# Kernel tuning notes

Hardware: AMD Instinct MI355X
Metric: run time of the kernel (lower is better)

Reference implementation:

```python
import jax, jax.numpy as jnp
from jax import lax
import numpy as np


def _gru_layer(x_seq, W_ih, W_hh, b_ih, b_hh):
    """Single GRU layer, torch gate ordering (r, z, n). x_seq: [B, T, I].
    Returns (all hidden states [B, T, H], final hidden [B, H])."""
    B, T, _ = x_seq.shape
    H = W_hh.shape[1]
    # Precompute input projections for all timesteps: [B, T, 3H]
    x_proj = jnp.einsum('bti,gi->btg', x_seq, W_ih) + b_ih

    def step(h, xp):
        hp = h @ W_hh.T + b_hh                       # [B, 3H]
        xr, xz, xn = jnp.split(xp, 3, axis=-1)
        hr, hz, hn = jnp.split(hp, 3, axis=-1)
        r = jax.nn.sigmoid(xr + hr)
        z = jax.nn.sigmoid(xz + hz)
        n = jnp.tanh(xn + r * hn)
        h_new = (1.0 - z) * n + z * h
        return h_new, h_new

    h0 = jnp.zeros((B, H), dtype=x_seq.dtype)
    hT, hs = lax.scan(step, h0, x_proj.transpose(1, 0, 2))  # scan over time
    return hs.transpose(1, 0, 2), hT


def setup_inputs() -> dict:
    key = jax.random.key(0)
    ks = jax.random.split(key, 12)
    B, T, I, H, O = 128, 1000, 64, 512, 1
    s_in = 1.0 / np.sqrt(H)  # torch GRU init scale
    d = {
        'x': jax.random.normal(ks[0], (B, T, I), jnp.float32),
        'W_ih0': jax.random.uniform(ks[1], (3 * H, I), jnp.float32, -s_in, s_in),
        'W_hh0': jax.random.uniform(ks[2], (3 * H, H), jnp.float32, -s_in, s_in),
        'b_ih0': jax.random.uniform(ks[3], (3 * H,), jnp.float32, -s_in, s_in),
        'b_hh0': jax.random.uniform(ks[4], (3 * H,), jnp.float32, -s_in, s_in),
        'W_ih1': jax.random.uniform(ks[5], (3 * H, H), jnp.float32, -s_in, s_in),
        'W_hh1': jax.random.uniform(ks[6], (3 * H, H), jnp.float32, -s_in, s_in),
        'b_ih1': jax.random.uniform(ks[7], (3 * H,), jnp.float32, -s_in, s_in),
        'b_hh1': jax.random.uniform(ks[8], (3 * H,), jnp.float32, -s_in, s_in),
        'W_fc': jax.random.uniform(ks[9], (O, H), jnp.float32, -s_in, s_in),
        'b_fc': jax.random.uniform(ks[10], (O,), jnp.float32, -s_in, s_in),
    }
    return d


def reference(x, W_ih0, W_hh0, b_ih0, b_hh0, W_ih1, W_hh1, b_ih1, b_hh1, W_fc, b_fc):
    # Layer 0 (eval mode: inter-layer dropout is identity)
    h_seq0, _ = _gru_layer(x, W_ih0, W_hh0, b_ih0, b_hh0)
    # Layer 1; final hidden state of the last layer is h_n[-1]
    _, hT1 = _gru_layer(h_seq0, W_ih1, W_hh1, b_ih1, b_hh1)
    out = hT1 @ W_fc.T + b_fc          # [B, O]
    return jax.nn.sigmoid(out)
```

## Files before the change

kernel.cpp:

```cpp
#include <hip/hip_runtime.h>

typedef unsigned int u32;
typedef unsigned short u16;
typedef short bf16x8 __attribute__((ext_vector_type(8)));
typedef float f32x4 __attribute__((ext_vector_type(4)));

#define TLEN 1000
#define BATCH 128
#define IDIM 64
#define HDIM 512

#define NWG 256
#define NTHR 256

#define H0_OFF 0
#define H1_OFF 262144
#define PX0_OFF 525312
#define PH0_OFF 721920
#define PX1_OFF 2294784
#define PH1_OFF 3867648
#define FLG_OFF 5440512
#define XSL_OFF 5442560

__device__ __forceinline__ u16 f2bf(float f) {
  u32 u = __float_as_uint(f);
  u += 0x7fffu + ((u >> 16) & 1u);
  return (u16)(u >> 16);
}
__device__ __forceinline__ float bf2f(u16 h) { return __uint_as_float(((u32)h) << 16); }
__device__ __forceinline__ float sigm(float x) { return 1.0f / (1.0f + __expf(-x)); }
__device__ __forceinline__ float tanhfast(float x) {
  float e = __expf(-2.0f * fabsf(x));
  float t = (1.0f - e) / (1.0f + e);
  return x >= 0.0f ? t : -t;
}
__device__ __forceinline__ u32 umin2(u32 a, u32 b) { return a < b ? a : b; }
__device__ __forceinline__ u32 umax2(u32 a, u32 b) { return a > b ? a : b; }

__device__ __forceinline__ void sys_st16(u16* p, u32 v) {
  asm volatile("global_store_short %0, %1, off sc0 sc1" ::"v"(p), "v"(v) : "memory");
}
__device__ __forceinline__ void sys_st32(u32* p, u32 v) {
  asm volatile("global_store_dword %0, %1, off sc0 sc1" ::"v"(p), "v"(v) : "memory");
}
__device__ __forceinline__ uint4 sys_ld128(const u32* p) {
  uint4 v;
  asm volatile("global_load_dwordx4 %0, %1, off sc0 sc1\n\ts_waitcnt vmcnt(0)"
               : "=v"(v) : "v"(p) : "memory");
  return v;
}
__device__ __forceinline__ void sys_ldA(bf16x8& d, const u16* p) {
  asm volatile("global_load_dwordx4 %0, %1, off sc0 sc1" : "=v"(d) : "v"(p));
}
__device__ __forceinline__ void dev_st32(u32* p, u32 v) {
  asm volatile("global_store_dword %0, %1, off sc1" ::"v"(p), "v"(v) : "memory");
}
__device__ __forceinline__ uint4 dev_ld128(const u32* p) {
  uint4 v;
  asm volatile("global_load_dwordx4 %0, %1, off sc1\n\ts_waitcnt vmcnt(0)"
               : "=v"(v) : "v"(p) : "memory");
  return v;
}
__device__ __forceinline__ void l2_st16(u16* p, u32 v) {
  asm volatile("global_store_short %0, %1, off sc0" ::"v"(p), "v"(v) : "memory");
}
__device__ __forceinline__ void l2_ldA(bf16x8& d, const u16* p) {
  asm volatile("global_load_dwordx4 %0, %1, off sc0" : "=v"(d) : "v"(p));
}

__global__ void pack_weights(const float* Wih0, const float* Whh0,
                             const float* Wih1, const float* Whh1, char* ws) {
  int fid = blockIdx.x * NTHR + threadIdx.x;
  const float* src;
  int K, Kks;
  size_t obase;
  int f = fid;
  if (f < 12288) {
    src = Wih0; K = 64; Kks = 2; obase = PX0_OFF;
  } else if (f < 12288 + 98304) {
    f -= 12288; src = Whh0; K = 512; Kks = 16; obase = PH0_OFF;
  } else if (f < 12288 + 2 * 98304) {
    f -= 12288 + 98304; src = Wih1; K = 512; Kks = 16; obase = PX1_OFF;
  } else if (f < 12288 + 3 * 98304) {
    f -= 12288 + 2 * 98304; src = Whh1; K = 512; Kks = 16; obase = PH1_OFF;
  } else {
    return;
  }
  int lane = f & 63;
  int r = f >> 6;
  int ks = r % Kks; r /= Kks;
  int ct = r % 3;
  int sl = r / 3;
  int grow = ct * 512 + sl * 16 + (lane & 15);
  int k = ks * 32 + ((lane >> 4) * 8);
  const float* s = src + (size_t)grow * K + k;
  u32 p0 = f2bf(s[0]) | ((u32)f2bf(s[1]) << 16);
  u32 p1 = f2bf(s[2]) | ((u32)f2bf(s[3]) << 16);
  u32 p2 = f2bf(s[4]) | ((u32)f2bf(s[5]) << 16);
  u32 p3 = f2bf(s[6]) | ((u32)f2bf(s[7]) << 16);
  *(uint4*)(ws + obase + (size_t)f * 16) = make_uint4(p0, p1, p2, p3);
}

__device__ __forceinline__ void fast_barrier(u32* flagsS, u32* flagsD, int fidx, u32 target) {
  __syncthreads();
  if (threadIdx.x == 0) {
    asm volatile("s_waitcnt vmcnt(0)" ::: "memory");
    dev_st32(flagsD + fidx, target);
    sys_st32(flagsS + fidx, target);
  }
  if (threadIdx.x < 64) {
    const int lane = threadIdx.x;
    for (;;) {
      u32 m = 0xFFFFFFFFu;
      if (lane < 8) {
        uint4 v = sys_ld128(flagsS + lane * 4);
        m = umin2(umin2(v.x, v.y), umin2(v.z, v.w));
      } else if (lane < 16) {
        uint4 v = dev_ld128(flagsD + (lane - 8) * 4);
        m = umin2(umin2(v.x, v.y), umin2(v.z, v.w));
      }
      m = umax2(m, __shfl_xor(m, 8));
      m = umin2(m, __shfl_xor(m, 1));
      m = umin2(m, __shfl_xor(m, 2));
      m = umin2(m, __shfl_xor(m, 4));
      if (__shfl(m, 0) >= target) break;
      __builtin_amdgcn_s_sleep(2);
    }
  }
  __syncthreads();
}

struct KP {
  const float *x, *bih0, *bhh0, *bih1, *bhh1, *Wfc, *bfc;
  float* out;
  char* ws;
};

#define MFMA(A, B, C) __builtin_amdgcn_mfma_f32_16x16x32_bf16((A), (B), (C), 0, 0, 0)

__global__ __launch_bounds__(NTHR, 1) void gru_main(KP P) {
  __shared__ f32x4 red[4][8][64];
  const int tid = threadIdx.x;
  const int lane = tid & 63;
  const int w = tid >> 6;
  const int b = blockIdx.x;
  const int bg = b & 7;
  const int q = b >> 3;
  const int layer = q & 1;
  const int colWG = q >> 1;

  char* ws = P.ws;
  u16* h0 = (u16*)(ws + H0_OFF);
  u16* h1 = (u16*)(ws + H1_OFF);
  u32* flagsS = (u32*)(ws + FLG_OFF) + bg * 64;
  u32* xslot = (u32*)(ws + XSL_OFF) + bg * 64;
  u32* flagsD = xslot + 32;
  const bf16x8* px = (const bf16x8*)(ws + (layer ? PX1_OFF : PX0_OFF));
  const bf16x8* ph = (const bf16x8*)(ws + (layer ? PH1_OFF : PH0_OFF));

  const float* bih = layer ? P.bih1 : P.bih0;
  const float* bhh = layer ? P.bhh1 : P.bhh0;
  const int cw = w & 1;
  const int jcol = colWG * 32 + cw * 16 + (lane & 15);
  const float b_r = bih[jcol] + bhh[jcol];
  const float b_z = bih[HDIM + jcol] + bhh[HDIM + jcol];
  const float b_nx = bih[2 * HDIM + jcol];
  const float b_nh = bhh[2 * HDIM + jcol];

  u16* hout = layer ? h1 : h0;
  const size_t bgoff = (size_t)bg * 16 * HDIM;

  bf16x8 xB[3][2][4], hB[3][2][4];
#pragma unroll
  for (int ct = 0; ct < 3; ++ct)
#pragma unroll
    for (int cs = 0; cs < 2; ++cs)
#pragma unroll
      for (int j = 0; j < 4; ++j)
        hB[ct][cs][j] =
            ph[((size_t)((colWG * 2 + cs) * 3 + ct) * 16 + (j * 4 + w)) * 64 + lane];
  if (layer == 0) {
    const bf16x8 z8 = {0, 0, 0, 0, 0, 0, 0, 0};
#pragma unroll
    for (int ct = 0; ct < 3; ++ct)
#pragma unroll
      for (int cs = 0; cs < 2; ++cs)
#pragma unroll
        for (int j = 0; j < 4; ++j) xB[ct][cs][j] = z8;
    if (w < 2) {
#pragma unroll
      for (int ct = 0; ct < 3; ++ct)
#pragma unroll
        for (int cs = 0; cs < 2; ++cs)
          xB[ct][cs][0] = px[((size_t)((colWG * 2 + cs) * 3 + ct) * 2 + w) * 64 + lane];
    }
  } else {
#pragma unroll
    for (int ct = 0; ct < 3; ++ct)
#pragma unroll
      for (int cs = 0; cs < 2; ++cs)
#pragma unroll
        for (int j = 0; j < 4; ++j)
          xB[ct][cs][j] =
              px[((size_t)((colWG * 2 + cs) * 3 + ct) * 16 + (j * 4 + w)) * 64 + lane];
  }

  u32 xcc = 0;
  asm volatile("s_getreg_b32 %0, hwreg(HW_REG_XCC_ID)" : "=s"(xcc));
  if (tid == 0) sys_st32(xslot + q, xcc + 1u);
  fast_barrier(flagsS, flagsD, q, 1u);
  u32 mn = 0xFFFFFFFFu, mx = 0u;
  if (lane < 8) {
    uint4 v = sys_ld128(xslot + lane * 4);
    mn = umin2(umin2(v.x, v.y), umin2(v.z, v.w));
    mx = umax2(umax2(v.x, v.y), umax2(v.z, v.w));
  }
  mn = umin2(mn, __shfl_xor(mn, 1)); mx = umax2(mx, __shfl_xor(mx, 1));
  mn = umin2(mn, __shfl_xor(mn, 2)); mx = umax2(mx, __shfl_xor(mx, 2));
  mn = umin2(mn, __shfl_xor(mn, 4)); mx = umax2(mx, __shfl_xor(mx, 4));
  mn = __shfl(mn, 0); mx = __shfl(mx, 0);
  const bool isLocal = (mn != 0u) && (mn == mx);

  const f32x4 zf = {0.f, 0.f, 0.f, 0.f};
  f32x4 hown = zf;

#pragma unroll 1
  for (int tick = 0; tick <= TLEN; ++tick) {
    const int p = tick & 1;
    const bool active = (layer == 0) ? (tick < TLEN) : (tick >= 1);
    if (active) {
      f32x4 aR[2], aZ[2], aXN[2], aHN[2];
#pragma unroll
      for (int cs = 0; cs < 2; ++cs) { aR[cs] = zf; aZ[cs] = zf; aXN[cs] = zf; aHN[cs] = zf; }
      const u16* h0src = h0 + (size_t)(1 - p) * BATCH * HDIM + bgoff;

      if (layer == 0) {
        if (w < 2) {
          const float* s = P.x +
              ((size_t)(bg * 16 + (lane & 15)) * TLEN + tick) * IDIM +
              w * 32 + ((lane >> 4) * 8);
          float4 v0 = ((const float4*)s)[0];
          float4 v1 = ((const float4*)s)[1];
          bf16x8 A;
          A[0] = (short)f2bf(v0.x); A[1] = (short)f2bf(v0.y);
          A[2] = (short)f2bf(v0.z); A[3] = (short)f2bf(v0.w);
          A[4] = (short)f2bf(v1.x); A[5] = (short)f2bf(v1.y);
          A[6] = (short)f2bf(v1.z); A[7] = (short)f2bf(v1.w);
#pragma unroll
          for (int cs = 0; cs < 2; ++cs) {
            aR[cs] = MFMA(A, xB[0][cs][0], aR[cs]);
            aZ[cs] = MFMA(A, xB[1][cs][0], aZ[cs]);
            aXN[cs] = MFMA(A, xB[2][cs][0], aXN[cs]);
          }
        }
        bf16x8 A[4];
        if (isLocal) {
#pragma unroll
          for (int j = 0; j < 4; ++j)
            l2_ldA(A[j], h0src + (size_t)(lane & 15) * HDIM + (j * 4 + w) * 32 +
                             ((lane >> 4) * 8));
        } else {
#pragma unroll
          for (int j = 0; j < 4; ++j)
            sys_ldA(A[j], h0src + (size_t)(lane & 15) * HDIM + (j * 4 + w) * 32 +
                              ((lane >> 4) * 8));
        }
        asm volatile("s_waitcnt vmcnt(0)" ::: "memory");
        __builtin_amdgcn_sched_barrier(0);
#pragma unroll
        for (int j = 0; j < 4; ++j)
#pragma unroll
          for (int cs = 0; cs < 2; ++cs) {
            aR[cs] = MFMA(A[j], hB[0][cs][j], aR[cs]);
            aZ[cs] = MFMA(A[j], hB[1][cs][j], aZ[cs]);
            aHN[cs] = MFMA(A[j], hB[2][cs][j], aHN[cs]);
          }
      } else {
        const u16* h1src = h1 + (size_t)(1 - p) * BATCH * HDIM + bgoff;
        bf16x8 A1[4], A2[4];
        if (isLocal) {
#pragma unroll
          for (int j = 0; j < 4; ++j) {
            const size_t off = (size_t)(lane & 15) * HDIM + (j * 4 + w) * 32 +
                               ((lane >> 4) * 8);
            l2_ldA(A1[j], h0src + off);
            l2_ldA(A2[j], h1src + off);
          }
        } else {
#pragma unroll
          for (int j = 0; j < 4; ++j) {
            const size_t off = (size_t)(lane & 15) * HDIM + (j * 4 + w) * 32 +
                               ((lane >> 4) * 8);
            sys_ldA(A1[j], h0src + off);
            sys_ldA(A2[j], h1src + off);
          }
        }
        asm volatile("s_waitcnt vmcnt(0)" ::: "memory");
        __builtin_amdgcn_sched_barrier(0);
#pragma unroll
        for (int j = 0; j < 4; ++j)
#pragma unroll
          for (int cs = 0; cs < 2; ++cs) {
            aR[cs] = MFMA(A1[j], xB[0][cs][j], aR[cs]);
            aZ[cs] = MFMA(A1[j], xB[1][cs][j], aZ[cs]);
            aXN[cs] = MFMA(A1[j], xB[2][cs][j], aXN[cs]);
          }
#pragma unroll
        for (int j = 0; j < 4; ++j)
#pragma unroll
          for (int cs = 0; cs < 2; ++cs) {
            aR[cs] = MFMA(A2[j], hB[0][cs][j], aR[cs]);
            aZ[cs] = MFMA(A2[j], hB[1][cs][j], aZ[cs]);
            aHN[cs] = MFMA(A2[j], hB[2][cs][j], aHN[cs]);
          }
      }

#pragma unroll
      for (int cs = 0; cs < 2; ++cs) {
        red[w][0 + cs][lane] = aR[cs];
        red[w][2 + cs][lane] = aZ[cs];
        red[w][4 + cs][lane] = aXN[cs];
        red[w][6 + cs][lane] = aHN[cs];
      }
      __syncthreads();
      f32x4 R = zf, Z = zf, XN = zf, HN = zf;
#pragma unroll
      for (int kq = 0; kq < 4; ++kq) {
        R = R + red[kq][0 + cw][lane];
        Z = Z + red[kq][2 + cw][lane];
        XN = XN + red[kq][4 + cw][lane];
        HN = HN + red[kq][6 + cw][lane];
      }

      if (w < 2) {
        u16* hw = hout + (size_t)p * BATCH * HDIM;
        u32 hv16[4];
        int rowb[4];
#pragma unroll
        for (int qq = 0; qq < 4; ++qq) {
          float r = sigm(R[qq] + b_r);
          float z = sigm(Z[qq] + b_z);
          float n = tanhfast(XN[qq] + b_nx + r * (HN[qq] + b_nh));
          float hv = (1.f - z) * n + z * hown[qq];
          hown[qq] = hv;
          hv16[qq] = (u32)f2bf(hv);
          rowb[qq] = bg * 16 + (lane >> 4) * 4 + qq;
        }
        if (isLocal) {
#pragma unroll
          for (int qq = 0; qq < 4; ++qq)
            l2_st16(&hw[(size_t)rowb[qq] * HDIM + jcol], hv16[qq]);
        } else {
#pragma unroll
          for (int qq = 0; qq < 4; ++qq)
            sys_st16(&hw[(size_t)rowb[qq] * HDIM + jcol], hv16[qq]);
        }
      }
    }
    fast_barrier(flagsS, flagsD, q, (u32)(tick + 2));
  }

  if (layer == 1 && colWG == 0) {
    const u16* hT = h1;
    int row = tid >> 4, qq = tid & 15;
    const u16* hr = hT + (size_t)(bg * 16 + row) * HDIM + qq * 32;
    bf16x8 hv[4];
    if (isLocal) {
#pragma unroll
      for (int c = 0; c < 4; ++c) l2_ldA(hv[c], hr + c * 8);
    } else {
#pragma unroll
      for (int c = 0; c < 4; ++c) sys_ldA(hv[c], hr + c * 8);
    }
    asm volatile("s_waitcnt vmcnt(0)" ::: "memory");
    const float* wf = P.Wfc + qq * 32;
    float s = 0.f;
#pragma unroll
    for (int c = 0; c < 4; ++c)
#pragma unroll
      for (int k = 0; k < 8; ++k) s += bf2f((u16)hv[c][k]) * wf[c * 8 + k];
    s += __shfl_xor(s, 1);
    s += __shfl_xor(s, 2);
    s += __shfl_xor(s, 4);
    s += __shfl_xor(s, 8);
    if (qq == 0) P.out[bg * 16 + row] = sigm(s + P.bfc[0]);
  }
}

extern "C" void kernel_launch(void* const* d_in, const int* in_sizes, int n_in,
                              void* d_out, int out_size, void* d_ws, size_t ws_size,
                              hipStream_t stream) {
  const float* x = (const float*)d_in[0];
  const float* Wih0 = (const float*)d_in[1];
  const float* Whh0 = (const float*)d_in[2];
  const float* bih0 = (const float*)d_in[3];
  const float* bhh0 = (const float*)d_in[4];
  const float* Wih1 = (const float*)d_in[5];
  const float* Whh1 = (const float*)d_in[6];
  const float* bih1 = (const float*)d_in[7];
  const float* bhh1 = (const float*)d_in[8];
  const float* Wfc = (const float*)d_in[9];
  const float* bfc = (const float*)d_in[10];

  hipMemsetAsync(d_ws, 0, 524288, stream);
  hipMemsetAsync((char*)d_ws + FLG_OFF, 0, 4096, stream);
  pack_weights<<<dim3(1200), dim3(NTHR), 0, stream>>>(Wih0, Whh0, Wih1, Whh1, (char*)d_ws);

  KP P = {x, bih0, bhh0, bih1, bhh1, Wfc, bfc, (float*)d_out, (char*)d_ws};
  void* args[] = {&P};
  hipError_t ce = hipLaunchCooperativeKernel((void*)gru_main, dim3(NWG), dim3(NTHR), args, 0,
                                             stream);
  if (ce != hipSuccess) {
    (void)hipGetLastError();
    gru_main<<<dim3(NWG), dim3(NTHR), 0, stream>>>(P);
  }
}
```

Baseline: 4.031 ms.

## Replace per-tick group barrier with per-producer progress flags and 4-slot hidden ring

Result: faster. 3.876 ms (-3.8%).

```diff
diff --git a/kernel.cpp b/kernel.cpp
--- a/kernel.cpp
+++ b/kernel.cpp
@@ -14,13 +14,13 @@
 #define NTHR 256
 
 #define H0_OFF 0
-#define H1_OFF 262144
-#define PX0_OFF 525312
-#define PH0_OFF 721920
-#define PX1_OFF 2294784
-#define PH1_OFF 3867648
-#define FLG_OFF 5440512
-#define XSL_OFF 5442560
+#define H1_OFF 524288
+#define PX0_OFF 1048576
+#define PH0_OFF 1245184
+#define PX1_OFF 2818048
+#define PH1_OFF 4390912
+#define FLG_OFF 5963776
+#define XSL_OFF 5967872
 
 __device__ __forceinline__ u16 f2bf(float f) {
   u32 u = __float_as_uint(f);
@@ -52,17 +52,17 @@
 __device__ __forceinline__ void sys_ldA(bf16x8& d, const u16* p) {
   asm volatile("global_load_dwordx4 %0, %1, off sc0 sc1" : "=v"(d) : "v"(p));
 }
-__device__ __forceinline__ void dev_st32(u32* p, u32 v) {
-  asm volatile("global_store_dword %0, %1, off sc1" ::"v"(p), "v"(v) : "memory");
-}
-__device__ __forceinline__ uint4 dev_ld128(const u32* p) {
+__device__ __forceinline__ void l2_st16(u16* p, u32 v) {
+  asm volatile("global_store_short %0, %1, off sc0" ::"v"(p), "v"(v) : "memory");
+}
+__device__ __forceinline__ void l2_st32(u32* p, u32 v) {
+  asm volatile("global_store_dword %0, %1, off sc0" ::"v"(p), "v"(v) : "memory");
+}
+__device__ __forceinline__ uint4 l2_ld128(const u32* p) {
   uint4 v;
-  asm volatile("global_load_dwordx4 %0, %1, off sc1\n\ts_waitcnt vmcnt(0)"
+  asm volatile("global_load_dwordx4 %0, %1, off sc0\n\ts_waitcnt vmcnt(0)"
                : "=v"(v) : "v"(p) : "memory");
   return v;
-}
-__device__ __forceinline__ void l2_st16(u16* p, u32 v) {
-  asm volatile("global_store_short %0, %1, off sc0" ::"v"(p), "v"(v) : "memory");
 }
 __device__ __forceinline__ void l2_ldA(bf16x8& d, const u16* p) {
   asm volatile("global_load_dwordx4 %0, %1, off sc0" : "=v"(d) : "v"(p));
@@ -101,35 +101,6 @@
   *(uint4*)(ws + obase + (size_t)f * 16) = make_uint4(p0, p1, p2, p3);
 }
 
-__device__ __forceinline__ void fast_barrier(u32* flagsS, u32* flagsD, int fidx, u32 target) {
-  __syncthreads();
-  if (threadIdx.x == 0) {
-    asm volatile("s_waitcnt vmcnt(0)" ::: "memory");
-    dev_st32(flagsD + fidx, target);
-    sys_st32(flagsS + fidx, target);
-  }
-  if (threadIdx.x < 64) {
-    const int lane = threadIdx.x;
-    for (;;) {
-      u32 m = 0xFFFFFFFFu;
-      if (lane < 8) {
-        uint4 v = sys_ld128(flagsS + lane * 4);
-        m = umin2(umin2(v.x, v.y), umin2(v.z, v.w));
-      } else if (lane < 16) {
-        uint4 v = dev_ld128(flagsD + (lane - 8) * 4);
-        m = umin2(umin2(v.x, v.y), umin2(v.z, v.w));
-      }
-      m = umax2(m, __shfl_xor(m, 8));
-      m = umin2(m, __shfl_xor(m, 1));
-      m = umin2(m, __shfl_xor(m, 2));
-      m = umin2(m, __shfl_xor(m, 4));
-      if (__shfl(m, 0) >= target) break;
-      __builtin_amdgcn_s_sleep(2);
-    }
-  }
-  __syncthreads();
-}
-
 struct KP {
   const float *x, *bih0, *bhh0, *bih1, *bhh1, *Wfc, *bfc;
   float* out;
@@ -137,6 +108,37 @@
 };
 
 #define MFMA(A, B, C) __builtin_amdgcn_mfma_f32_16x16x32_bf16((A), (B), (C), 0, 0, 0)
+
+__device__ __forceinline__ void wait_flags(const u32* fl0s, const u32* fl1s,
+                                           const u32* fl0f, const u32* fl1f,
+                                           u32 bias, u32 k) {
+  if (threadIdx.x < 64) {
+    const int lane = threadIdx.x;
+    for (;;) {
+      u32 m = 0xFFFFFFFFu;
+      if (lane < 4) {
+        uint4 v = sys_ld128(fl0s + lane * 4);
+        m = umin2(umin2(v.x, v.y), umin2(v.z, v.w));
+      } else if (lane < 8) {
+        uint4 v = sys_ld128(fl1s + (lane - 4) * 4);
+        m = umin2(umin2(v.x, v.y), umin2(v.z, v.w)) + bias;
+      } else if (lane < 12) {
+        uint4 v = l2_ld128(fl0f + (lane - 8) * 4);
+        m = umin2(umin2(v.x, v.y), umin2(v.z, v.w));
+      } else if (lane < 16) {
+        uint4 v = l2_ld128(fl1f + (lane - 12) * 4);
+        m = umin2(umin2(v.x, v.y), umin2(v.z, v.w)) + bias;
+      }
+      m = umax2(m, __shfl_xor(m, 8));
+      m = umin2(m, __shfl_xor(m, 4));
+      m = umin2(m, __shfl_xor(m, 2));
+      m = umin2(m, __shfl_xor(m, 1));
+      if (__shfl(m, 0) >= k) break;
+      __builtin_amdgcn_s_sleep(1);
+    }
+  }
+  __syncthreads();
+}
 
 __global__ __launch_bounds__(NTHR, 1) void gru_main(KP P) {
   __shared__ f32x4 red[4][8][64];
@@ -152,11 +154,18 @@
   char* ws = P.ws;
   u16* h0 = (u16*)(ws + H0_OFF);
   u16* h1 = (u16*)(ws + H1_OFF);
-  u32* flagsS = (u32*)(ws + FLG_OFF) + bg * 64;
-  u32* xslot = (u32*)(ws + XSL_OFF) + bg * 64;
-  u32* flagsD = xslot + 32;
+  u32* fb = (u32*)(ws + FLG_OFF) + bg * 128;
+  u32* fl0s = fb;
+  u32* fl1s = fb + 32;
+  u32* fl0f = fb + 64;
+  u32* fl1f = fb + 96;
+  u32* xsl = (u32*)(ws + XSL_OFF) + bg * 64;
+  u32* phf = xsl + 32;
   const bf16x8* px = (const bf16x8*)(ws + (layer ? PX1_OFF : PX0_OFF));
   const bf16x8* ph = (const bf16x8*)(ws + (layer ? PH1_OFF : PH0_OFF));
+
+  u32* mySig_s = (layer ? fl1s : fl0s) + colWG;
+  u32* mySig_f = (layer ? fl1f : fl0f) + colWG;
 
   const float* bih = layer ? P.bih1 : P.bih0;
   const float* bhh = layer ? P.bhh1 : P.bhh0;
@@ -167,8 +176,8 @@
   const float b_nx = bih[2 * HDIM + jcol];
   const float b_nh = bhh[2 * HDIM + jcol];
 
-  u16* hout = layer ? h1 : h0;
   const size_t bgoff = (size_t)bg * 16 * HDIM;
+  const size_t SLOT = (size_t)BATCH * HDIM;
 
   bf16x8 xB[3][2][4], hB[3][2][4];
 #pragma unroll
@@ -207,11 +216,27 @@
 
   u32 xcc = 0;
   asm volatile("s_getreg_b32 %0, hwreg(HW_REG_XCC_ID)" : "=s"(xcc));
-  if (tid == 0) sys_st32(xslot + q, xcc + 1u);
-  fast_barrier(flagsS, flagsD, q, 1u);
+  if (tid == 0) sys_st32(xsl + q, xcc + 1u);
+  __syncthreads();
+  if (tid == 0) sys_st32(phf + q, 1u);
+  if (tid < 64) {
+    for (;;) {
+      u32 m = 0xFFFFFFFFu;
+      if (lane < 8) {
+        uint4 v = sys_ld128(phf + lane * 4);
+        m = umin2(umin2(v.x, v.y), umin2(v.z, v.w));
+      }
+      m = umin2(m, __shfl_xor(m, 1));
+      m = umin2(m, __shfl_xor(m, 2));
+      m = umin2(m, __shfl_xor(m, 4));
+      if (__shfl(m, 0) >= 1u) break;
+      __builtin_amdgcn_s_sleep(2);
+    }
+  }
+  __syncthreads();
   u32 mn = 0xFFFFFFFFu, mx = 0u;
   if (lane < 8) {
-    uint4 v = sys_ld128(xslot + lane * 4);
+    uint4 v = sys_ld128(xsl + lane * 4);
     mn = umin2(umin2(v.x, v.y), umin2(v.z, v.w));
     mx = umax2(umax2(v.x, v.y), umax2(v.z, v.w));
   }
@@ -225,19 +250,18 @@
   f32x4 hown = zf;
 
 #pragma unroll 1
-  for (int tick = 0; tick <= TLEN; ++tick) {
-    const int p = tick & 1;
-    const bool active = (layer == 0) ? (tick < TLEN) : (tick >= 1);
+  for (int k = 0; k <= TLEN; ++k) {
+    const bool active = (layer == 0) ? (k < TLEN) : (k >= 1);
     if (active) {
       f32x4 aR[2], aZ[2], aXN[2], aHN[2];
 #pragma unroll
       for (int cs = 0; cs < 2; ++cs) { aR[cs] = zf; aZ[cs] = zf; aXN[cs] = zf; aHN[cs] = zf; }
-      const u16* h0src = h0 + (size_t)(1 - p) * BATCH * HDIM + bgoff;
+      const u16* h0src = h0 + (size_t)((k + 3) & 3) * SLOT + bgoff;
 
       if (layer == 0) {
         if (w < 2) {
           const float* s = P.x +
-              ((size_t)(bg * 16 + (lane & 15)) * TLEN + tick) * IDIM +
+              ((size_t)(bg * 16 + (lane & 15)) * TLEN + k) * IDIM +
               w * 32 + ((lane >> 4) * 8);
           float4 v0 = ((const float4*)s)[0];
           float4 v1 = ((const float4*)s)[1];
@@ -253,6 +277,7 @@
             aXN[cs] = MFMA(A, xB[2][cs][0], aXN[cs]);
           }
         }
+        if (k > 0) wait_flags(fl0s, fl1s, fl0f, fl1f, 2u, (u32)k);
         bf16x8 A[4];
         if (isLocal) {
 #pragma unroll
@@ -276,7 +301,8 @@
             aHN[cs] = MFMA(A[j], hB[2][cs][j], aHN[cs]);
           }
       } else {
-        const u16* h1src = h1 + (size_t)(1 - p) * BATCH * HDIM + bgoff;
+        wait_flags(fl0s, fl1s, fl0f, fl1f, 1u, (u32)k);
+        const u16* h1src = h1 + (size_t)((k + 2) & 3) * SLOT + bgoff;
         bf16x8 A1[4], A2[4];
         if (isLocal) {
 #pragma unroll
@@ -331,9 +357,11 @@
         XN = XN + red[kq][4 + cw][lane];
         HN = HN + red[kq][6 + cw][lane];
       }
+      __syncthreads();
 
       if (w < 2) {
-        u16* hw = hout + (size_t)p * BATCH * HDIM;
+        u16* hw = (layer ? h1 + (size_t)((k + 3) & 3) * SLOT
+                         : h0 + (size_t)(k & 3) * SLOT);
         u32 hv16[4];
         int rowb[4];
 #pragma unroll
@@ -356,12 +384,36 @@
             sys_st16(&hw[(size_t)rowb[qq] * HDIM + jcol], hv16[qq]);
         }
       }
-    }
-    fast_barrier(flagsS, flagsD, q, (u32)(tick + 2));
+
+      __syncthreads();
+      if (tid == 0) {
+        asm volatile("s_waitcnt vmcnt(0)" ::: "memory");
+        l2_st32(mySig_f, (u32)(k + 1));
+        sys_st32(mySig_s, (u32)(k + 1));
+      }
+    }
   }
 
   if (layer == 1 && colWG == 0) {
-    const u16* hT = h1;
+    if (tid < 64) {
+      for (;;) {
+        u32 m = 0xFFFFFFFFu;
+        if (lane < 4) {
+          uint4 v = sys_ld128(fl1s + lane * 4);
+          m = umin2(umin2(v.x, v.y), umin2(v.z, v.w));
+        } else if (lane < 8) {
+          uint4 v = l2_ld128(fl1f + (lane - 4) * 4);
+          m = umin2(umin2(v.x, v.y), umin2(v.z, v.w));
+        }
+        m = umax2(m, __shfl_xor(m, 4));
+        m = umin2(m, __shfl_xor(m, 1));
+        m = umin2(m, __shfl_xor(m, 2));
+        if (__shfl(m, 0) >= (u32)(TLEN + 1)) break;
+        __builtin_amdgcn_s_sleep(1);
+      }
+    }
+    __syncthreads();
+    const u16* hT = h1 + (size_t)((TLEN + 3) & 3) * SLOT;
     int row = tid >> 4, qq = tid & 15;
     const u16* hr = hT + (size_t)(bg * 16 + row) * HDIM + qq * 32;
     bf16x8 hv[4];
@@ -378,7 +430,7 @@
 #pragma unroll
     for (int c = 0; c < 4; ++c)
 #pragma unroll
-      for (int k = 0; k < 8; ++k) s += bf2f((u16)hv[c][k]) * wf[c * 8 + k];
+      for (int k2 = 0; k2 < 8; ++k2) s += bf2f((u16)hv[c][k2]) * wf[c * 8 + k2];
     s += __shfl_xor(s, 1);
     s += __shfl_xor(s, 2);
     s += __shfl_xor(s, 4);
@@ -402,8 +454,8 @@
   const float* Wfc = (const float*)d_in[9];
   const float* bfc = (const float*)d_in[10];
 
-  hipMemsetAsync(d_ws, 0, 524288, stream);
-  hipMemsetAsync((char*)d_ws + FLG_OFF, 0, 4096, stream);
+  hipMemsetAsync(d_ws, 0, 1048576, stream);
+  hipMemsetAsync((char*)d_ws + FLG_OFF, 0, 6144, stream);
   pack_weights<<<dim3(1200), dim3(NTHR), 0, stream>>>(Wih0, Whh0, Wih1, Whh1, (char*)d_ws);
 
   KP P = {x, bih0, bhh0, bih1, bhh1, Wfc, bfc, (float*)d_out, (char*)d_ws};
```
